# Kernel optimization log

Measured on AMD Instinct MI355X. Metric: run time of the kernel, lower is better.

The kernel has to match this reference:

```python
import jax, jax.numpy as jnp
import numpy as np

N_NODES = 50000
N_EDGES = 800000
F_IN = 24
H = 128
N_GRAPHS = 100
BN_EPS = 1e-5


def setup_inputs() -> dict:
    key = jax.random.key(0)
    ks = jax.random.split(key, 12)
    x = jax.random.normal(ks[0], (N_NODES, F_IN), dtype=jnp.float32)
    edge_index = jax.random.randint(ks[1], (2, N_EDGES), 0, N_NODES, dtype=jnp.int32)
    batch = (jnp.arange(N_NODES, dtype=jnp.int32) // (N_NODES // N_GRAPHS)).astype(jnp.int32)

    def lin(k, fan_in, fan_out):
        bound = 1.0 / np.sqrt(fan_in)
        kw, kb = jax.random.split(k)
        W = jax.random.uniform(kw, (fan_in, fan_out), jnp.float32, -bound, bound)
        b = jax.random.uniform(kb, (fan_out,), jnp.float32, -bound, bound)
        return W, b

    W1, b1 = lin(ks[2], 2 * F_IN, H)
    W2, b2 = lin(ks[3], 2 * H, H)
    W3, b3 = lin(ks[4], 2 * H, H)
    Wl, bl = lin(ks[5], H, 1)
    g1 = jnp.ones((H,), jnp.float32); be1 = jnp.zeros((H,), jnp.float32)
    g2 = jnp.ones((H,), jnp.float32); be2 = jnp.zeros((H,), jnp.float32)
    g3 = jnp.ones((H,), jnp.float32); be3 = jnp.zeros((H,), jnp.float32)
    return {"x": x, "edge_index": edge_index, "batch": batch,
            "W1": W1, "b1": b1, "W2": W2, "b2": b2, "W3": W3, "b3": b3,
            "g1": g1, "be1": be1, "g2": g2, "be2": be2, "g3": g3, "be3": be3,
            "Wl": Wl, "bl": bl}


def edge_conv(x, src, dst, W, b):
    # PyG EdgeConv: message = mlp([x_i, x_j - x_i]) for edge j->i, aggr=max at i
    x_i = x[dst]                                    # [E, F]
    e = jnp.concatenate([x_i, x[src] - x_i], axis=-1)  # [E, 2F]
    m = jax.nn.relu(e @ W + b)                      # [E, H]
    out = jax.ops.segment_max(m, dst, num_segments=N_NODES)
    return jnp.where(jnp.isfinite(out), out, 0.0)   # isolated nodes -> 0


def batch_norm(h, g, b):
    # training-mode BN over node dim (biased variance), dropout treated as identity
    mu = h.mean(axis=0)
    var = ((h - mu) ** 2).mean(axis=0)
    return g * (h - mu) * jax.lax.rsqrt(var + BN_EPS) + b


def reference(x, edge_index, batch, W1, b1, W2, b2, W3, b3,
              g1, be1, g2, be2, g3, be3, Wl, bl):
    src, dst = edge_index[0], edge_index[1]
    h = edge_conv(x, src, dst, W1, b1)
    h = jax.nn.relu(batch_norm(h, g1, be1))
    h = edge_conv(h, src, dst, W2, b2)
    h = jax.nn.relu(batch_norm(h, g2, be2))
    h = edge_conv(h, src, dst, W3, b3)
    h = batch_norm(h, g3, be3)
    # global_mean_pool
    sums = jax.ops.segment_sum(h, batch, num_segments=N_GRAPHS)           # [G, H]
    counts = jax.ops.segment_sum(jnp.ones((h.shape[0],), h.dtype), batch,
                                 num_segments=N_GRAPHS)
    pooled = sums / jnp.maximum(counts, 1.0)[:, None]
    return jax.nn.relu(pooled @ Wl + bl)                                  # [G, 1]
```

## Files before the change

### kernel.cpp

```cpp
#include <hip/hip_runtime.h>

#define N_NODES 50000
#define N_EDGES 800000
#define F_IN 24
#define HDIM 128
#define N_GRAPHS 100
#define BN_EPS 1e-5f
#define NBLK 196
#define ROWS_PER_GRAPH (N_NODES / N_GRAPHS)
#define MM_GRID 782
#define HIST_BLKS ((N_EDGES + 255) / 256)
#define PREP_BLKS (F_IN + 2 * HDIM)
#define SSTR 32
#define SUMS_PER_LAYER (256 * SSTR)
#define STATS_BLKS 196

typedef _Float16 h2 __attribute__((ext_vector_type(2)));
typedef _Float16 f16x8 __attribute__((ext_vector_type(8)));
typedef float f32x4 __attribute__((ext_vector_type(4)));

template <int K, int KC>
__global__ __launch_bounds__(256) void k_mm1(const float* __restrict__ X,
                                             const float* __restrict__ Wcat,
                                             const float* __restrict__ bias,
                                             float* __restrict__ A, _Float16* __restrict__ C) {
    __shared__ float Xs[KC * 68];
    __shared__ float Ws[KC * 128];
    int tid = threadIdx.x;
    int row0 = blockIdx.x * 64;
    const bool isA = (blockIdx.y == 0);
    const int colbase = isA ? 0 : 128;
    int cg = tid & 31;
    int rg = tid >> 5;

    float acc[8][4];
#pragma unroll
    for (int ri = 0; ri < 8; ++ri)
#pragma unroll
        for (int ci = 0; ci < 4; ++ci)
            acc[ri][ci] = isA ? bias[cg * 4 + ci] : 0.f;

    for (int k0 = 0; k0 < K; k0 += KC) {
        __syncthreads();
        {
            const int C4 = KC / 4;
            for (int i = tid; i < 64 * C4; i += 256) {
                int c4 = i % C4, r = i / C4;
                int row = row0 + r;
                float4 v = make_float4(0.f, 0.f, 0.f, 0.f);
                if (row < N_NODES) v = *(const float4*)&X[row * K + k0 + c4 * 4];
                Xs[(c4 * 4 + 0) * 68 + r] = v.x;
                Xs[(c4 * 4 + 1) * 68 + r] = v.y;
                Xs[(c4 * 4 + 2) * 68 + r] = v.z;
                Xs[(c4 * 4 + 3) * 68 + r] = v.w;
            }
        }
        for (int i = tid; i < KC * 32; i += 256) {
            int c4 = i & 31, kr = i >> 5;
            *(float4*)&Ws[kr * 128 + c4 * 4] =
                *(const float4*)&Wcat[(k0 + kr) * 256 + colbase + c4 * 4];
        }
        __syncthreads();
#pragma unroll
        for (int kk = 0; kk < KC; ++kk) {
            float4 t0 = *(const float4*)&Xs[kk * 68 + rg * 8];
            float4 t1 = *(const float4*)&Xs[kk * 68 + rg * 8 + 4];
            float4 w = *(const float4*)&Ws[kk * 128 + cg * 4];
            float t[8] = {t0.x, t0.y, t0.z, t0.w, t1.x, t1.y, t1.z, t1.w};
            float wv[4] = {w.x, w.y, w.z, w.w};
#pragma unroll
            for (int ri = 0; ri < 8; ++ri)
#pragma unroll
                for (int ci = 0; ci < 4; ++ci)
                    acc[ri][ci] += t[ri] * wv[ci];
        }
    }

#pragma unroll
    for (int ri = 0; ri < 8; ++ri) {
        int row = row0 + rg * 8 + ri;
        if (row < N_NODES) {
            if (isA) {
                *(float4*)&A[row * HDIM + cg * 4] =
                    make_float4(acc[ri][0], acc[ri][1], acc[ri][2], acc[ri][3]);
            } else {
                union { h2 h[2]; uint2 u; } pk;
                pk.h[0] = h2{(_Float16)acc[ri][0], (_Float16)acc[ri][1]};
                pk.h[1] = h2{(_Float16)acc[ri][2], (_Float16)acc[ri][3]};
                *(uint2*)&C[row * HDIM + cg * 4] = pk.u;
            }
        }
    }
}

__global__ __launch_bounds__(256) void k_mmf(const float* __restrict__ X,
                                             const _Float16* __restrict__ Wf,
                                             const float* __restrict__ bias,
                                             const float* __restrict__ sums,
                                             const float* __restrict__ g,
                                             const float* __restrict__ be,
                                             float* __restrict__ A, _Float16* __restrict__ C) {
    __shared__ _Float16 Xh[16 * 520];
    __shared__ _Float16 Wh[128 * 128];
    __shared__ float scs[128], shs[128];
    int tid = threadIdx.x;
    int lane = tid & 63, wv = tid >> 6;
    int row0 = blockIdx.x * 64;
    const bool isA = (blockIdx.y == 0);
    const _Float16* Wsrc = Wf + (isA ? 0 : 16384);

    if (tid < 128) {
        float S  = sums[tid * SSTR];
        float S2 = sums[(128 + tid) * SSTR];
        float mean = S / (float)N_NODES;
        float var = fmaxf(S2 / (float)N_NODES - mean * mean, 0.f);
        float scv = g[tid] / sqrtf(var + BN_EPS);
        scs[tid] = scv;
        shs[tid] = be[tid] - mean * scv;
    }
    {
        const uint4* s = (const uint4*)Wsrc;
        uint4* d = (uint4*)Wh;
        for (int i = tid; i < 2048; i += 256) d[i] = s[i];
    }
    __syncthreads();
    for (int i = tid; i < 64 * 32; i += 256) {
        int k4 = i & 31, rl = i >> 5;
        int row = row0 + rl;
        float4 v = make_float4(0.f, 0.f, 0.f, 0.f);
        if (row < N_NODES) v = *(const float4*)&X[row * HDIM + k4 * 4];
        int c = k4 * 4;
        v.x = fmaxf(v.x * scs[c + 0] + shs[c + 0], 0.f);
        v.y = fmaxf(v.y * scs[c + 1] + shs[c + 1], 0.f);
        v.z = fmaxf(v.z * scs[c + 2] + shs[c + 2], 0.f);
        v.w = fmaxf(v.w * scs[c + 3] + shs[c + 3], 0.f);
        int rt = rl >> 4, m = rl & 15, kc = k4 >> 3, q = (k4 >> 1) & 3, jh = k4 & 1;
        _Float16* d = Xh + (rt * 4 + kc) * 520 + (q * 16 + m) * 8 + jh * 4;
        d[0] = (_Float16)v.x; d[1] = (_Float16)v.y;
        d[2] = (_Float16)v.z; d[3] = (_Float16)v.w;
    }
    __syncthreads();

    int n = lane & 15, q = lane >> 4;
    f32x4 acc[8];
#pragma unroll
    for (int nt = 0; nt < 8; ++nt) {
        float b0 = isA ? bias[nt * 16 + n] : 0.f;
        acc[nt] = f32x4{b0, b0, b0, b0};
    }
#pragma unroll
    for (int kc = 0; kc < 4; ++kc) {
        f16x8 a = *(const f16x8*)(Xh + (wv * 4 + kc) * 520 + lane * 8);
#pragma unroll
        for (int nt = 0; nt < 8; ++nt) {
            f16x8 b = *(const f16x8*)(Wh + ((nt * 4 + kc) * 64 + lane) * 8);
            acc[nt] = __builtin_amdgcn_mfma_f32_16x16x32_f16(a, b, acc[nt], 0, 0, 0);
        }
    }
#pragma unroll
    for (int nt = 0; nt < 8; ++nt) {
#pragma unroll
        for (int r = 0; r < 4; ++r) {
            int row = row0 + wv * 16 + q * 4 + r;
            if (row < N_NODES) {
                int col = nt * 16 + n;
                if (isA) A[row * HDIM + col] = acc[nt][r];
                else     C[row * HDIM + col] = (_Float16)acc[nt][r];
            }
        }
    }
}

__global__ void k_pre(const float* __restrict__ W1, const float* __restrict__ W2,
                      const float* __restrict__ W3, float* __restrict__ Wcat1,
                      _Float16* __restrict__ Wf2, _Float16* __restrict__ Wf3,
                      const int* __restrict__ dst, unsigned* __restrict__ deg,
                      unsigned* __restrict__ rank) {
    int b = blockIdx.x;
    int j = threadIdx.x;
    if (b < F_IN) {
        float wb = W1[(b + F_IN) * HDIM + (j & 127)];
        float wt = W1[b * HDIM + (j & 127)];
        Wcat1[b * 256 + j] = (j < HDIM) ? (wt - wb) : wb;
    } else if (b < PREP_BLKS) {
        int idx = b - F_IN;
        int layer = idx >> 7;
        int k = idx & 127;
        const float* W = layer ? W3 : W2;
        _Float16* Wf   = layer ? Wf3 : Wf2;
        int col = j & 127;
        float wt = W[k * HDIM + col];
        float wb = W[(k + HDIM) * HDIM + col];
        float v = (j < 128) ? (wt - wb) : wb;
        int plane = j >> 7;
        int nt = col >> 4, n = col & 15, kc = k >> 5, q = (k >> 3) & 3, jj = k & 7;
        int f = ((nt * 4 + kc) * 4 + q) * 128 + n * 8 + jj;
        Wf[plane * 16384 + f] = (_Float16)v;
    } else {
        int e = (b - PREP_BLKS) * 256 + j;
        if (e < N_EDGES) rank[e] = atomicAdd(&deg[dst[e]], 1u);
    }
}

__global__ __launch_bounds__(256) void k_scanall(const unsigned* __restrict__ deg,
                                                 unsigned* __restrict__ bsum,
                                                 unsigned* __restrict__ off) {
    __shared__ unsigned s[256];
    int t = threadIdx.x;
    int b = blockIdx.x;
    int i = b * 256 + t;
    unsigned v = (i < N_NODES) ? deg[i] : 0u;
    s[t] = v;
    __syncthreads();
    for (int d = 1; d < 256; d <<= 1) {
        unsigned u = (t >= d) ? s[t - d] : 0u;
        __syncthreads();
        s[t] += u;
        __syncthreads();
    }
    unsigned locex = s[t] - v;
    if (t == 255) atomicExch(&bsum[b], s[255] + 1u);
    __syncthreads();
    unsigned bs = 0;
    if (t < NBLK) {
        unsigned x;
        do { x = atomicAdd(&bsum[t], 0u); } while (x == 0u);
        bs = x - 1u;
    }
    s[t] = (t < NBLK) ? bs : 0u;
    __syncthreads();
    for (int d = 1; d < 256; d <<= 1) {
        unsigned u = (t >= d) ? s[t - d] : 0u;
        __syncthreads();
        s[t] += u;
        __syncthreads();
    }
    unsigned bexcl = (b == 0) ? 0u : s[b - 1];
    if (i < N_NODES) off[i] = bexcl + locex;
}

__global__ void k_scatter(const int* __restrict__ src, const int* __restrict__ dst,
                          const unsigned* __restrict__ off, const unsigned* __restrict__ rank,
                          unsigned* __restrict__ ssrc) {
    int e = blockIdx.x * 256 + threadIdx.x;
    if (e < N_EDGES)
        ssrc[off[dst[e]] + rank[e]] = (unsigned)src[e];
}

__global__ __launch_bounds__(256) void k_agg(const float* __restrict__ A,
                                             const h2* __restrict__ Cc,
                                             const unsigned* __restrict__ off,
                                             const unsigned* __restrict__ deg,
                                             const unsigned* __restrict__ ssrc,
                                             float* __restrict__ H) {
    __shared__ unsigned sl[4][64];
    int w = threadIdx.x >> 6;
    int lane = threadIdx.x & 63;
    int i = blockIdx.x * 4 + w;
    int d = (int)deg[i];
    unsigned o = off[i];
    union { unsigned short us[2]; h2 v; } ninf;
    ninf.us[0] = 0xFC00; ninf.us[1] = 0xFC00;
    h2 m2 = ninf.v;
    for (int base = 0; base < d; base += 64) {
        int cntc = min(64, d - base);
        if (lane < cntc) sl[w][lane] = ssrc[o + base + lane];
        int e = 0;
        for (; e + 8 <= cntc; e += 8) {
            unsigned s0 = sl[w][e + 0], s1 = sl[w][e + 1], s2 = sl[w][e + 2], s3 = sl[w][e + 3];
            unsigned s4 = sl[w][e + 4], s5 = sl[w][e + 5], s6 = sl[w][e + 6], s7 = sl[w][e + 7];
            h2 v0 = Cc[s0 * 64 + lane];
            h2 v1 = Cc[s1 * 64 + lane];
            h2 v2 = Cc[s2 * 64 + lane];
            h2 v3 = Cc[s3 * 64 + lane];
            h2 v4 = Cc[s4 * 64 + lane];
            h2 v5 = Cc[s5 * 64 + lane];
            h2 v6 = Cc[s6 * 64 + lane];
            h2 v7 = Cc[s7 * 64 + lane];
            h2 a0 = __builtin_elementwise_max(v0, v1);
            h2 a1 = __builtin_elementwise_max(v2, v3);
            h2 a2 = __builtin_elementwise_max(v4, v5);
            h2 a3 = __builtin_elementwise_max(v6, v7);
            h2 b0 = __builtin_elementwise_max(a0, a1);
            h2 b1 = __builtin_elementwise_max(a2, a3);
            m2 = __builtin_elementwise_max(m2, __builtin_elementwise_max(b0, b1));
        }
        if (e + 4 <= cntc) {
            unsigned s0 = sl[w][e + 0], s1 = sl[w][e + 1], s2 = sl[w][e + 2], s3 = sl[w][e + 3];
            h2 v0 = Cc[s0 * 64 + lane];
            h2 v1 = Cc[s1 * 64 + lane];
            h2 v2 = Cc[s2 * 64 + lane];
            h2 v3 = Cc[s3 * 64 + lane];
            h2 a0 = __builtin_elementwise_max(v0, v1);
            h2 a1 = __builtin_elementwise_max(v2, v3);
            m2 = __builtin_elementwise_max(m2, __builtin_elementwise_max(a0, a1));
            e += 4;
        }
        for (; e < cntc; ++e)
            m2 = __builtin_elementwise_max(m2, Cc[sl[w][e] * 64 + lane]);
    }
    float2 a = *(const float2*)&A[i * HDIM + lane * 2];
    float2 hv;
    hv.x = (d > 0) ? fmaxf(a.x + (float)m2.x, 0.f) : 0.f;
    hv.y = (d > 0) ? fmaxf(a.y + (float)m2.y, 0.f) : 0.f;
    *(float2*)&H[i * HDIM + lane * 2] = hv;
}

__global__ __launch_bounds__(256) void k_stats(const float* __restrict__ H,
                                               float* __restrict__ sums) {
    __shared__ float4 ls[256], ls2[256];
    int t = threadIdx.x;
    int c4 = t & 31, rg = t >> 5;
    int row0 = blockIdx.x * 256;
    float4 s = make_float4(0.f, 0.f, 0.f, 0.f);
    float4 s2 = make_float4(0.f, 0.f, 0.f, 0.f);
#pragma unroll 4
    for (int it = 0; it < 32; ++it) {
        int row = row0 + rg * 32 + it;
        if (row < N_NODES) {
            float4 v = *(const float4*)&H[row * HDIM + c4 * 4];
            s.x += v.x; s.y += v.y; s.z += v.z; s.w += v.w;
            s2.x += v.x * v.x; s2.y += v.y * v.y; s2.z += v.z * v.z; s2.w += v.w * v.w;
        }
    }
    ls[t] = s; ls2[t] = s2;
    __syncthreads();
    if (t < 32) {
        float4 a = ls[t], a2 = ls2[t];
#pragma unroll
        for (int j = 1; j < 8; ++j) {
            float4 b = ls[j * 32 + t], b2 = ls2[j * 32 + t];
            a.x += b.x; a.y += b.y; a.z += b.z; a.w += b.w;
            a2.x += b2.x; a2.y += b2.y; a2.z += b2.z; a2.w += b2.w;
        }
        int c = t * 4;
        atomicAdd(&sums[(c + 0) * SSTR], a.x);
        atomicAdd(&sums[(c + 1) * SSTR], a.y);
        atomicAdd(&sums[(c + 2) * SSTR], a.z);
        atomicAdd(&sums[(c + 3) * SSTR], a.w);
        atomicAdd(&sums[(128 + c + 0) * SSTR], a2.x);
        atomicAdd(&sums[(128 + c + 1) * SSTR], a2.y);
        atomicAdd(&sums[(128 + c + 2) * SSTR], a2.z);
        atomicAdd(&sums[(128 + c + 3) * SSTR], a2.w);
    }
}

__global__ __launch_bounds__(128) void k_poolout(const float* __restrict__ H,
                                                 const float* __restrict__ sums,
                                                 const float* __restrict__ g,
                                                 const float* __restrict__ be,
                                                 const float* __restrict__ Wl,
                                                 const float* __restrict__ bl,
                                                 float* __restrict__ out) {
    int gi = blockIdx.x;
    int k = threadIdx.x;
    float S  = sums[k * SSTR];
    float S2 = sums[(128 + k) * SSTR];
    float mean = S / (float)N_NODES;
    float var = fmaxf(S2 / (float)N_NODES - mean * mean, 0.f);
    float scv = g[k] / sqrtf(var + BN_EPS);
    float shv = be[k] - mean * scv;
    const float* base = H + (size_t)gi * ROWS_PER_GRAPH * HDIM;
    float s = 0.f;
#pragma unroll 4
    for (int r = 0; r < ROWS_PER_GRAPH; ++r) s += base[r * HDIM + k];
    float pb = scv * (s * (1.f / (float)ROWS_PER_GRAPH)) + shv;
    float p = pb * Wl[k];
    __shared__ float red[2];
    for (int o = 32; o > 0; o >>= 1) p += __shfl_down(p, o);
    if ((k & 63) == 0) red[k >> 6] = p;
    __syncthreads();
    if (k == 0) out[gi] = fmaxf(red[0] + red[1] + bl[0], 0.f);
}

extern "C" void kernel_launch(void* const* d_in, const int* in_sizes, int n_in,
                              void* d_out, int out_size, void* d_ws, size_t ws_size,
                              hipStream_t stream) {
    const float* x   = (const float*)d_in[0];
    const int* ei    = (const int*)d_in[1];
    const float* W1  = (const float*)d_in[3];
    const float* b1  = (const float*)d_in[4];
    const float* W2  = (const float*)d_in[5];
    const float* b2  = (const float*)d_in[6];
    const float* W3  = (const float*)d_in[7];
    const float* b3  = (const float*)d_in[8];
    const float* g1  = (const float*)d_in[9];
    const float* be1 = (const float*)d_in[10];
    const float* g2  = (const float*)d_in[11];
    const float* be2 = (const float*)d_in[12];
    const float* g3  = (const float*)d_in[13];
    const float* be3 = (const float*)d_in[14];
    const float* Wl  = (const float*)d_in[15];
    const float* bl  = (const float*)d_in[16];
    float* out = (float*)d_out;

    const int* srcp = ei;
    const int* dstp = ei + N_EDGES;

    char* ws = (char*)d_ws;
    size_t o = 0;
    auto alloc = [&](size_t bytes) -> void* {
        o = (o + 255) & ~(size_t)255;
        void* p = ws + o;
        o += bytes;
        return p;
    };
    float* A      = (float*)alloc((size_t)N_NODES * HDIM * 4);
    _Float16* C   = (_Float16*)alloc((size_t)N_NODES * HDIM * 2);
    float* h      = (float*)alloc((size_t)N_NODES * HDIM * 4);
    float* Wcat1  = (float*)alloc((size_t)F_IN * 256 * 4);
    _Float16* Wf2 = (_Float16*)alloc((size_t)2 * 16384 * 2);
    _Float16* Wf3 = (_Float16*)alloc((size_t)2 * 16384 * 2);
    unsigned* deg  = (unsigned*)alloc((size_t)N_NODES * 4);
    unsigned* bsum = (unsigned*)alloc((size_t)NBLK * 4);
    float* sums    = (float*)alloc((size_t)3 * SUMS_PER_LAYER * 4);
    unsigned* off  = (unsigned*)alloc((size_t)N_NODES * 4);
    unsigned* rank = (unsigned*)alloc((size_t)N_EDGES * 4);
    unsigned* ssrc = (unsigned*)alloc((size_t)N_EDGES * 4);
    (void)ws_size; (void)n_in; (void)in_sizes; (void)out_size;

    float* sums0 = sums;
    float* sums1 = sums + SUMS_PER_LAYER;
    float* sums2 = sums + 2 * SUMS_PER_LAYER;

    size_t zlen = (size_t)((char*)(sums + 3 * SUMS_PER_LAYER) - (char*)deg);
    (void)hipMemsetAsync(deg, 0, zlen, stream);

    k_pre<<<PREP_BLKS + HIST_BLKS, 256, 0, stream>>>(W1, W2, W3, Wcat1, Wf2, Wf3,
                                                     dstp, deg, rank);
    k_scanall<<<NBLK, 256, 0, stream>>>(deg, bsum, off);
    k_scatter<<<HIST_BLKS, 256, 0, stream>>>(srcp, dstp, off, rank, ssrc);

    const dim3 MMG(MM_GRID, 2);
    const int AGB = N_NODES / 4;

    k_mm1<F_IN, F_IN><<<MMG, 256, 0, stream>>>(x, Wcat1, b1, A, C);
    k_agg<<<AGB, 256, 0, stream>>>(A, (const h2*)C, off, deg, ssrc, h);
    k_stats<<<STATS_BLKS, 256, 0, stream>>>(h, sums0);

    k_mmf<<<MMG, 256, 0, stream>>>(h, Wf2, b2, sums0, g1, be1, A, C);
    k_agg<<<AGB, 256, 0, stream>>>(A, (const h2*)C, off, deg, ssrc, h);
    k_stats<<<STATS_BLKS, 256, 0, stream>>>(h, sums1);

    k_mmf<<<MMG, 256, 0, stream>>>(h, Wf3, b3, sums1, g2, be2, A, C);
    k_agg<<<AGB, 256, 0, stream>>>(A, (const h2*)C, off, deg, ssrc, h);
    k_stats<<<STATS_BLKS, 256, 0, stream>>>(h, sums2);

    k_poolout<<<N_GRAPHS, 128, 0, stream>>>(h, sums2, g3, be3, Wl, bl, out);
}
```

Before: 408.9 us.

## Store hidden activations in fp16 and fuse final BN stats into pooling

The aggregated node features h are now written as fp16 instead of fp32, which halves the write traffic in k_agg and the read traffic in k_stats and k_mmf. The last k_stats pass is removed. A per-graph pooling kernel now accumulates column sums and sums of squares and atomically adds them into the BN statistics, and a single-block kernel applies BN and the linear head. This cuts memory traffic and one full pass over h. The cost is fp16 rounding of the pre-BN activations and a pooling kernel that runs only 100 blocks.

```diff
diff --git a/kernel.cpp b/kernel.cpp
--- a/kernel.cpp
+++ b/kernel.cpp
@@ -16,6 +16,7 @@
 #define STATS_BLKS 196
 
 typedef _Float16 h2 __attribute__((ext_vector_type(2)));
+typedef _Float16 h4 __attribute__((ext_vector_type(4)));
 typedef _Float16 f16x8 __attribute__((ext_vector_type(8)));
 typedef float f32x4 __attribute__((ext_vector_type(4)));
 
@@ -93,7 +94,7 @@
     }
 }
 
-__global__ __launch_bounds__(256) void k_mmf(const float* __restrict__ X,
+__global__ __launch_bounds__(256) void k_mmf(const _Float16* __restrict__ X,
                                              const _Float16* __restrict__ Wf,
                                              const float* __restrict__ bias,
                                              const float* __restrict__ sums,
@@ -128,7 +129,10 @@
         int k4 = i & 31, rl = i >> 5;
         int row = row0 + rl;
         float4 v = make_float4(0.f, 0.f, 0.f, 0.f);
-        if (row < N_NODES) v = *(const float4*)&X[row * HDIM + k4 * 4];
+        if (row < N_NODES) {
+            h4 xv = *(const h4*)&X[row * HDIM + k4 * 4];
+            v = make_float4((float)xv.x, (float)xv.y, (float)xv.z, (float)xv.w);
+        }
         int c = k4 * 4;
         v.x = fmaxf(v.x * scs[c + 0] + shs[c + 0], 0.f);
         v.y = fmaxf(v.y * scs[c + 1] + shs[c + 1], 0.f);
@@ -252,7 +256,7 @@
                                              const unsigned* __restrict__ off,
                                              const unsigned* __restrict__ deg,
                                              const unsigned* __restrict__ ssrc,
-                                             float* __restrict__ H) {
+                                             h2* __restrict__ H) {
     __shared__ unsigned sl[4][64];
     int w = threadIdx.x >> 6;
     int lane = threadIdx.x & 63;
@@ -300,13 +304,12 @@
             m2 = __builtin_elementwise_max(m2, Cc[sl[w][e] * 64 + lane]);
     }
     float2 a = *(const float2*)&A[i * HDIM + lane * 2];
-    float2 hv;
-    hv.x = (d > 0) ? fmaxf(a.x + (float)m2.x, 0.f) : 0.f;
-    hv.y = (d > 0) ? fmaxf(a.y + (float)m2.y, 0.f) : 0.f;
-    *(float2*)&H[i * HDIM + lane * 2] = hv;
-}
-
-__global__ __launch_bounds__(256) void k_stats(const float* __restrict__ H,
+    float hx = (d > 0) ? fmaxf(a.x + (float)m2.x, 0.f) : 0.f;
+    float hy = (d > 0) ? fmaxf(a.y + (float)m2.y, 0.f) : 0.f;
+    H[i * 64 + lane] = h2{(_Float16)hx, (_Float16)hy};
+}
+
+__global__ __launch_bounds__(256) void k_stats(const _Float16* __restrict__ H,
                                                float* __restrict__ sums) {
     __shared__ float4 ls[256], ls2[256];
     int t = threadIdx.x;
@@ -318,7 +321,8 @@
     for (int it = 0; it < 32; ++it) {
         int row = row0 + rg * 32 + it;
         if (row < N_NODES) {
-            float4 v = *(const float4*)&H[row * HDIM + c4 * 4];
+            h4 hv = *(const h4*)&H[row * HDIM + c4 * 4];
+            float4 v = make_float4((float)hv.x, (float)hv.y, (float)hv.z, (float)hv.w);
             s.x += v.x; s.y += v.y; s.z += v.z; s.w += v.w;
             s2.x += v.x * v.x; s2.y += v.y * v.y; s2.z += v.z * v.z; s2.w += v.w * v.w;
         }
@@ -345,32 +349,47 @@
     }
 }
 
-__global__ __launch_bounds__(128) void k_poolout(const float* __restrict__ H,
-                                                 const float* __restrict__ sums,
-                                                 const float* __restrict__ g,
-                                                 const float* __restrict__ be,
-                                                 const float* __restrict__ Wl,
-                                                 const float* __restrict__ bl,
-                                                 float* __restrict__ out) {
-    int gi = blockIdx.x;
+__global__ __launch_bounds__(128) void k_poolsum(const _Float16* __restrict__ H,
+                                                 float* __restrict__ Pg,
+                                                 float* __restrict__ sums) {
+    int g = blockIdx.x;
+    int k = threadIdx.x;
+    const _Float16* base = H + (size_t)g * ROWS_PER_GRAPH * HDIM;
+    float s = 0.f, s2 = 0.f;
+#pragma unroll 4
+    for (int r = 0; r < ROWS_PER_GRAPH; ++r) {
+        float v = (float)base[r * HDIM + k];
+        s += v; s2 += v * v;
+    }
+    Pg[g * HDIM + k] = s;
+    atomicAdd(&sums[k * SSTR], s);
+    atomicAdd(&sums[(128 + k) * SSTR], s2);
+}
+
+__global__ __launch_bounds__(128) void k_out(const float* __restrict__ Pg,
+                                             const float* __restrict__ sums,
+                                             const float* __restrict__ g3,
+                                             const float* __restrict__ be3,
+                                             const float* __restrict__ Wl,
+                                             const float* __restrict__ bl,
+                                             float* __restrict__ out) {
     int k = threadIdx.x;
     float S  = sums[k * SSTR];
     float S2 = sums[(128 + k) * SSTR];
     float mean = S / (float)N_NODES;
     float var = fmaxf(S2 / (float)N_NODES - mean * mean, 0.f);
-    float scv = g[k] / sqrtf(var + BN_EPS);
-    float shv = be[k] - mean * scv;
-    const float* base = H + (size_t)gi * ROWS_PER_GRAPH * HDIM;
-    float s = 0.f;
-#pragma unroll 4
-    for (int r = 0; r < ROWS_PER_GRAPH; ++r) s += base[r * HDIM + k];
-    float pb = scv * (s * (1.f / (float)ROWS_PER_GRAPH)) + shv;
-    float p = pb * Wl[k];
+    float scv = g3[k] / sqrtf(var + BN_EPS);
+    float shv = be3[k] - mean * scv;
+    float wk = Wl[k];
     __shared__ float red[2];
-    for (int o = 32; o > 0; o >>= 1) p += __shfl_down(p, o);
-    if ((k & 63) == 0) red[k >> 6] = p;
-    __syncthreads();
-    if (k == 0) out[gi] = fmaxf(red[0] + red[1] + bl[0], 0.f);
+    for (int g = 0; g < N_GRAPHS; ++g) {
+        float p = (scv * (Pg[g * HDIM + k] * (1.f / (float)ROWS_PER_GRAPH)) + shv) * wk;
+        for (int o = 32; o > 0; o >>= 1) p += __shfl_down(p, o);
+        if ((k & 63) == 0) red[k >> 6] = p;
+        __syncthreads();
+        if (k == 0) out[g] = fmaxf(red[0] + red[1] + bl[0], 0.f);
+        __syncthreads();
+    }
 }
 
 extern "C" void kernel_launch(void* const* d_in, const int* in_sizes, int n_in,
@@ -407,7 +426,7 @@
     };
     float* A      = (float*)alloc((size_t)N_NODES * HDIM * 4);
     _Float16* C   = (_Float16*)alloc((size_t)N_NODES * HDIM * 2);
-    float* h      = (float*)alloc((size_t)N_NODES * HDIM * 4);
+    _Float16* h   = (_Float16*)alloc((size_t)N_NODES * HDIM * 2);
     float* Wcat1  = (float*)alloc((size_t)F_IN * 256 * 4);
     _Float16* Wf2 = (_Float16*)alloc((size_t)2 * 16384 * 2);
     _Float16* Wf3 = (_Float16*)alloc((size_t)2 * 16384 * 2);
@@ -417,6 +436,7 @@
     unsigned* off  = (unsigned*)alloc((size_t)N_NODES * 4);
     unsigned* rank = (unsigned*)alloc((size_t)N_EDGES * 4);
     unsigned* ssrc = (unsigned*)alloc((size_t)N_EDGES * 4);
+    float* Pg      = (float*)alloc((size_t)N_GRAPHS * HDIM * 4);
     (void)ws_size; (void)n_in; (void)in_sizes; (void)out_size;
 
     float* sums0 = sums;
@@ -435,16 +455,16 @@
     const int AGB = N_NODES / 4;
 
     k_mm1<F_IN, F_IN><<<MMG, 256, 0, stream>>>(x, Wcat1, b1, A, C);
-    k_agg<<<AGB, 256, 0, stream>>>(A, (const h2*)C, off, deg, ssrc, h);
+    k_agg<<<AGB, 256, 0, stream>>>(A, (const h2*)C, off, deg, ssrc, (h2*)h);
     k_stats<<<STATS_BLKS, 256, 0, stream>>>(h, sums0);
 
     k_mmf<<<MMG, 256, 0, stream>>>(h, Wf2, b2, sums0, g1, be1, A, C);
-    k_agg<<<AGB, 256, 0, stream>>>(A, (const h2*)C, off, deg, ssrc, h);
+    k_agg<<<AGB, 256, 0, stream>>>(A, (const h2*)C, off, deg, ssrc, (h2*)h);
     k_stats<<<STATS_BLKS, 256, 0, stream>>>(h, sums1);
 
     k_mmf<<<MMG, 256, 0, stream>>>(h, Wf3, b3, sums1, g2, be2, A, C);
-    k_agg<<<AGB, 256, 0, stream>>>(A, (const h2*)C, off, deg, ssrc, h);
-    k_stats<<<STATS_BLKS, 256, 0, stream>>>(h, sums2);
-
-    k_poolout<<<N_GRAPHS, 128, 0, stream>>>(h, sums2, g3, be3, Wl, bl, out);
-}
+    k_agg<<<AGB, 256, 0, stream>>>(A, (const h2*)C, off, deg, ssrc, (h2*)h);
+
+    k_poolsum<<<N_GRAPHS, 128, 0, stream>>>(h, Pg, sums2);
+    k_out<<<1, 128, 0, stream>>>(Pg, sums2, g3, be3, Wl, bl, out);
+}
```

New measurement: 450.1 us. 10.1% more time.
